# Kernel optimization log

Hardware: AMD Instinct MI355X
Metric: run time of the kernel (lower is better)

Reference implementation:

```python
import jax, jax.numpy as jnp
import numpy as np

B, S, VOCAB, HID, NH, L, SPAN = 4, 512, 25, 512, 8, 12, 512
HEAD = HID // NH
FF = 4 * HID
EPS = 1e-7  # DebertaV2 layer_norm_eps


def _ln(x, g, b):
    m = x.mean(-1, keepdims=True)
    v = ((x - m) ** 2).mean(-1, keepdims=True)
    return (x - m) / jnp.sqrt(v + EPS) * g + b


def setup_inputs() -> dict:
    key = jax.random.key(0)
    ks = iter(jax.random.split(key, 16))
    w = lambda shape: jax.random.normal(next(ks), shape, jnp.float32) * 0.05
    return {
        "x": jax.random.randint(next(ks), (B, S), 0, VOCAB),
        "attention_mask": jnp.ones((B, S), jnp.int32),
        "word_emb": w((VOCAB, HID)),
        "emb_ln_g": jnp.ones((HID,), jnp.float32),
        "emb_ln_b": jnp.zeros((HID,), jnp.float32),
        "rel_emb": w((2 * SPAN, HID)),
        "Wq": w((L, HID, HID)), "bq": jnp.zeros((L, HID), jnp.float32),
        "Wk": w((L, HID, HID)), "bk": jnp.zeros((L, HID), jnp.float32),
        "Wv": w((L, HID, HID)), "bv": jnp.zeros((L, HID), jnp.float32),
        "Wpk": w((L, HID, HID)), "bpk": jnp.zeros((L, HID), jnp.float32),
        "Wpq": w((L, HID, HID)), "bpq": jnp.zeros((L, HID), jnp.float32),
        "Wo": w((L, HID, HID)), "bo": jnp.zeros((L, HID), jnp.float32),
        "ln1_g": jnp.ones((L, HID), jnp.float32), "ln1_b": jnp.zeros((L, HID), jnp.float32),
        "W1": w((L, HID, FF)), "b1": jnp.zeros((L, FF), jnp.float32),
        "W2": w((L, FF, HID)), "b2": jnp.zeros((L, HID), jnp.float32),
        "ln2_g": jnp.ones((L, HID), jnp.float32), "ln2_b": jnp.zeros((L, HID), jnp.float32),
        "cls_w": w((VOCAB, HID)), "cls_b": jnp.zeros((VOCAB,), jnp.float32),
    }


def _forward(x, attention_mask, word_emb, emb_ln_g, emb_ln_b, rel_emb,
             Wq, bq, Wk, bk, Wv, bv, Wpk, bpk, Wpq, bpq, Wo, bo,
             ln1_g, ln1_b, W1, b1, W2, b2, ln2_g, ln2_b, cls_w, cls_b):
    mask = attention_mask.astype(jnp.float32)
    # embeddings: word only (position_biased_input=False), LN, then masked
    h = _ln(word_emb[x], emb_ln_g, emb_ln_b) * mask[..., None]

    rel = jnp.arange(S)[:, None] - jnp.arange(S)[None, :]          # q_pos - k_pos
    c2p_idx = jnp.clip(rel + SPAN, 0, 2 * SPAN - 1)[None, None]    # [1,1,S,S]
    p2c_idx = jnp.clip(-rel + SPAN, 0, 2 * SPAN - 1)[None, None]
    attm = (mask[:, None, None, :] * mask[:, None, :, None]) > 0   # [B,1,S,S]
    scale = jnp.sqrt(jnp.float32(HEAD * 3))                        # scale_factor = 1 + len(pos_att_type)
    neg = jnp.finfo(jnp.float32).min

    def heads(t):  # [B,S,HID] -> [B,NH,S,HEAD]
        return t.reshape(B, S, NH, HEAD).transpose(0, 2, 1, 3)

    for l in range(L):
        q = heads(h @ Wq[l] + bq[l])
        k = heads(h @ Wk[l] + bk[l])
        v = heads(h @ Wv[l] + bv[l])
        # projected relative-position embeddings: [NH, 2*SPAN, HEAD]
        pk = (rel_emb @ Wpk[l] + bpk[l]).reshape(2 * SPAN, NH, HEAD).transpose(1, 0, 2)
        pq = (rel_emb @ Wpq[l] + bpq[l]).reshape(2 * SPAN, NH, HEAD).transpose(1, 0, 2)

        scores = jnp.einsum('bhqd,bhkd->bhqk', q, k)
        # c2p: query content vs key position, gathered at clamp(rel+span)
        c2p = jnp.take_along_axis(jnp.einsum('bhqd,hpd->bhqp', q, pk), c2p_idx, axis=-1)
        # p2c: key content vs query position, gathered at clamp(-rel+span) then transposed
        p2c = jnp.take_along_axis(jnp.einsum('bhkd,hpd->bhkp', k, pq), p2c_idx, axis=-1)
        scores = (scores + c2p + jnp.swapaxes(p2c, -1, -2)) / scale

        scores = jnp.where(attm, scores, neg)
        probs = jnp.where(attm, jax.nn.softmax(scores, axis=-1), 0.0)  # XSoftmax
        ctx = jnp.einsum('bhqk,bhkd->bhqd', probs, v).transpose(0, 2, 1, 3).reshape(B, S, HID)
        h = _ln(ctx @ Wo[l] + bo[l] + h, ln1_g[l], ln1_b[l])
        f = jax.nn.gelu(h @ W1[l] + b1[l], approximate=False) @ W2[l] + b2[l]
        h = _ln(f + h, ln2_g[l], ln2_b[l])

    logits = h @ cls_w.T + cls_b
    return h, logits


def reference(x, attention_mask, word_emb, emb_ln_g, emb_ln_b, rel_emb,
              Wq, bq, Wk, bk, Wv, bv, Wpk, bpk, Wpq, bpq, Wo, bo,
              ln1_g, ln1_b, W1, b1, W2, b2, ln2_g, ln2_b, cls_w, cls_b):
    return _forward(x, attention_mask, word_emb, emb_ln_g, emb_ln_b, rel_emb,
                    Wq, bq, Wk, bk, Wv, bv, Wpk, bpk, Wpq, bpq, Wo, bo,
                    ln1_g, ln1_b, W1, b1, W2, b2, ln2_g, ln2_b, cls_w, cls_b)
```

## Files before the change

### kernel.cpp

```cpp
#include <hip/hip_runtime.h>
#include <hip/hip_bf16.h>

#define BATCH  4
#define SEQ    512
#define TOK    (BATCH*SEQ)
#define HID    512
#define NHEAD  8
#define HEAD   64
#define FFDIM  2048
#define NLAYER 12
#define SPAN2  1024
#define VOCAB  25
#define LNEPS  1e-7f
#define NEG_BIG -3.0e38f

typedef __attribute__((ext_vector_type(8))) short bf16x8;
typedef __attribute__((ext_vector_type(4))) float floatx4;

#define MFMA16(a, b, c) __builtin_amdgcn_mfma_f32_16x16x32_bf16((a), (b), (c), 0, 0, 0)

__device__ __forceinline__ float b2f(unsigned short u) {
    return __uint_as_float(((unsigned int)u) << 16);
}
__device__ __forceinline__ unsigned short f2b(float f) {
    __hip_bfloat16 h = __float2bfloat16(f);
    return *(unsigned short*)&h;
}

__device__ __forceinline__ float block_reduce_sum(float v, float* red) {
    int tid = threadIdx.x;
    red[tid] = v; __syncthreads();
    for (int s = 128; s > 0; s >>= 1) { if (tid < s) red[tid] += red[tid + s]; __syncthreads(); }
    float r = red[0]; __syncthreads();
    return r;
}

__global__ void embed_ln_kernel(const int* __restrict__ x, const int* __restrict__ am,
                                const float* __restrict__ word_emb,
                                const float* __restrict__ g, const float* __restrict__ bb,
                                float* __restrict__ h, unsigned short* __restrict__ hb) {
    __shared__ float red[256];
    int t = blockIdx.x, tid = threadIdx.x;
    const float* we = word_emb + (size_t)x[t] * HID;
    float v1 = we[tid], v2 = we[tid + 256];
    float mean = block_reduce_sum(v1 + v2, red) * (1.0f / HID);
    float d1 = v1 - mean, d2 = v2 - mean;
    float var = block_reduce_sum(d1 * d1 + d2 * d2, red) * (1.0f / HID);
    float rstd = rsqrtf(var + LNEPS);
    float maskf = (float)am[t];
    size_t base = (size_t)t * HID;
    float o1 = (d1 * rstd * g[tid]       + bb[tid])       * maskf;
    float o2 = (d2 * rstd * g[tid + 256] + bb[tid + 256]) * maskf;
    h[base + tid] = o1;        h[base + tid + 256] = o2;
    hb[base + tid] = f2b(o1);  hb[base + tid + 256] = f2b(o2);
}

__global__ void add_ln_kernel(const float* __restrict__ tmp,
                              const float* __restrict__ g, const float* __restrict__ bb,
                              float* __restrict__ h, unsigned short* __restrict__ hb) {
    __shared__ float red[256];
    int t = blockIdx.x, tid = threadIdx.x;
    size_t base = (size_t)t * HID;
    float v1 = tmp[base + tid] + h[base + tid];
    float v2 = tmp[base + tid + 256] + h[base + tid + 256];
    float mean = block_reduce_sum(v1 + v2, red) * (1.0f / HID);
    float d1 = v1 - mean, d2 = v2 - mean;
    float var = block_reduce_sum(d1 * d1 + d2 * d2, red) * (1.0f / HID);
    float rstd = rsqrtf(var + LNEPS);
    float o1 = d1 * rstd * g[tid]       + bb[tid];
    float o2 = d2 * rstd * g[tid + 256] + bb[tid + 256];
    h[base + tid] = o1;        h[base + tid + 256] = o2;
    hb[base + tid] = f2b(o1);  hb[base + tid + 256] = f2b(o2);
}

__global__ void add_ln2_kernel(const float* __restrict__ t1a, const float* __restrict__ t1b,
                               const float* __restrict__ g, const float* __restrict__ bb,
                               float* __restrict__ h, unsigned short* __restrict__ hb) {
    __shared__ float red[256];
    int t = blockIdx.x, tid = threadIdx.x;
    size_t base = (size_t)t * HID;
    float v1 = t1a[base + tid] + t1b[base + tid] + h[base + tid];
    float v2 = t1a[base + tid + 256] + t1b[base + tid + 256] + h[base + tid + 256];
    float mean = block_reduce_sum(v1 + v2, red) * (1.0f / HID);
    float d1 = v1 - mean, d2 = v2 - mean;
    float var = block_reduce_sum(d1 * d1 + d2 * d2, red) * (1.0f / HID);
    float rstd = rsqrtf(var + LNEPS);
    float o1 = d1 * rstd * g[tid]       + bb[tid];
    float o2 = d2 * rstd * g[tid + 256] + bb[tid + 256];
    h[base + tid] = o1;        h[base + tid + 256] = o2;
    hb[base + tid] = f2b(o1);  hb[base + tid + 256] = f2b(o2);
}

__global__ void cvt_rel_kernel(const float* __restrict__ in, unsigned short* __restrict__ out) {
    int i = (blockIdx.x * 256 + threadIdx.x) * 4;
    float4 v = *(const float4*)(in + i);
    out[i] = f2b(v.x); out[i+1] = f2b(v.y); out[i+2] = f2b(v.z); out[i+3] = f2b(v.w);
}

__global__ void tcvt_kernel(const float* __restrict__ in, unsigned short* __restrict__ out,
                            int K, int N) {
    __shared__ float tile[32][33];
    int l = blockIdx.z;
    const float* ip = in + (size_t)l * K * N;
    unsigned short* op = out + (size_t)l * K * N;
    int kb = blockIdx.y * 32, nb = blockIdx.x * 32;
    int tx = threadIdx.x, ty = threadIdx.y;
    #pragma unroll
    for (int i = 0; i < 32; i += 8) tile[ty + i][tx] = ip[(size_t)(kb + ty + i) * N + nb + tx];
    __syncthreads();
    #pragma unroll
    for (int i = 0; i < 32; i += 8) op[(size_t)(nb + ty + i) * K + kb + tx] = f2b(tile[tx][ty + i]);
}

__global__ void tcvt6_kernel(const float* __restrict__ Wq, const float* __restrict__ Wk,
                             const float* __restrict__ Wv, const float* __restrict__ Wpk,
                             const float* __restrict__ Wpq, const float* __restrict__ Wo,
                             unsigned short* __restrict__ out) {
    __shared__ float tile[32][33];
    int z = blockIdx.z, l = z / 6, w = z - l * 6;
    const float* src = w == 0 ? Wq : w == 1 ? Wk : w == 2 ? Wv : w == 3 ? Wpk : w == 4 ? Wpq : Wo;
    const float* ip = src + (size_t)l * HID * HID;
    unsigned short* op = out + ((size_t)w * NLAYER + l) * HID * HID;
    int kb = blockIdx.y * 32, nb = blockIdx.x * 32;
    int tx = threadIdx.x, ty = threadIdx.y;
    #pragma unroll
    for (int i = 0; i < 32; i += 8) tile[ty + i][tx] = ip[(size_t)(kb + ty + i) * HID + nb + tx];
    __syncthreads();
    #pragma unroll
    for (int i = 0; i < 32; i += 8) op[(size_t)(nb + ty + i) * HID + kb + tx] = f2b(tile[tx][ty + i]);
}

__device__ __forceinline__ void gemm_tile_bt(
    const unsigned short* __restrict__ A, const unsigned short* __restrict__ Bt,
    int row0, int col0, int K, int kbeg, int kend,
    floatx4 (&acc)[2][2], unsigned short (&As)[64][72], unsigned short (&Bs)[64][72]) {
    int tid = threadIdx.x;
    int lane = tid & 63, wid = tid >> 6;
    int wm = wid >> 1, wn = wid & 1;
    int m16 = lane & 15, quad = lane >> 4;
    int sr = tid >> 2, sc = (tid & 3) << 4;
    const unsigned short* Ag = A + (size_t)(row0 + sr) * K + sc;
    const unsigned short* Bg = Bt + (size_t)(col0 + sr) * K + sc;
    for (int k0 = kbeg; k0 < kend; k0 += 64) {
        uint4 av0 = *(const uint4*)(Ag + k0);
        uint4 av1 = *(const uint4*)(Ag + k0 + 8);
        uint4 bv0 = *(const uint4*)(Bg + k0);
        uint4 bv1 = *(const uint4*)(Bg + k0 + 8);
        *(uint4*)&As[sr][sc]     = av0;
        *(uint4*)&As[sr][sc + 8] = av1;
        *(uint4*)&Bs[sr][sc]     = bv0;
        *(uint4*)&Bs[sr][sc + 8] = bv1;
        __syncthreads();
        #pragma unroll
        for (int kk = 0; kk < 2; kk++) {
            bf16x8 a0 = *(const bf16x8*)&As[wm * 32 + m16][kk * 32 + quad * 8];
            bf16x8 a1 = *(const bf16x8*)&As[wm * 32 + 16 + m16][kk * 32 + quad * 8];
            bf16x8 b0 = *(const bf16x8*)&Bs[wn * 32 + m16][kk * 32 + quad * 8];
            bf16x8 b1 = *(const bf16x8*)&Bs[wn * 32 + 16 + m16][kk * 32 + quad * 8];
            acc[0][0] = MFMA16(a0, b0, acc[0][0]);
            acc[0][1] = MFMA16(a0, b1, acc[0][1]);
            acc[1][0] = MFMA16(a1, b0, acc[1][0]);
            acc[1][1] = MFMA16(a1, b1, acc[1][1]);
        }
        __syncthreads();
    }
}

template<bool OUT_BF16, bool GELU, int SPLITK>
__global__ __launch_bounds__(256) void gemm_bt(
    const unsigned short* __restrict__ A, const unsigned short* __restrict__ Bt,
    const float* __restrict__ bias, void* __restrict__ Cp, int N, int K) {
    __shared__ unsigned short As[64][72], Bs[64][72];
    int row0 = blockIdx.y * 64, col0 = blockIdx.x * 64;
    int kseg = K / SPLITK;
    int kbeg = kseg * blockIdx.z, kend = kbeg + kseg;
    floatx4 acc[2][2];
    #pragma unroll
    for (int mi = 0; mi < 2; mi++)
        #pragma unroll
        for (int ni = 0; ni < 2; ni++) acc[mi][ni] = (floatx4){0.f, 0.f, 0.f, 0.f};
    gemm_tile_bt(A, Bt, row0, col0, K, kbeg, kend, acc, As, Bs);

    int tid = threadIdx.x, lane = tid & 63, wid = tid >> 6;
    int wm = wid >> 1, wn = wid & 1, m16 = lane & 15, quad = lane >> 4;
    size_t outoff = (size_t)blockIdx.z * (size_t)(gridDim.y << 6) * N;
    #pragma unroll
    for (int ni = 0; ni < 2; ni++) {
        int colg = col0 + wn * 32 + ni * 16 + m16;
        float bval = (SPLITK == 1 || blockIdx.z == 0) ? bias[colg] : 0.0f;
        #pragma unroll
        for (int mi = 0; mi < 2; mi++) {
            #pragma unroll
            for (int r = 0; r < 4; r++) {
                int rowg = row0 + wm * 32 + mi * 16 + quad * 4 + r;
                float v = acc[mi][ni][r] + bval;
                if (GELU) v = 0.5f * v * (1.0f + erff(v * 0.70710678118654752f));
                if (OUT_BF16) ((unsigned short*)Cp)[(size_t)rowg * N + colg] = f2b(v);
                else          ((float*)Cp)[outoff + (size_t)rowg * N + colg] = v;
            }
        }
    }
}

__global__ __launch_bounds__(256) void qkvp_gemm(
    const unsigned short* __restrict__ hb, const unsigned short* __restrict__ relb,
    const unsigned short* __restrict__ Wqt, const unsigned short* __restrict__ Wkt,
    const unsigned short* __restrict__ Wvt, const unsigned short* __restrict__ Wpkt,
    const unsigned short* __restrict__ Wpqt,
    const float* __restrict__ bq, const float* __restrict__ bk, const float* __restrict__ bv,
    const float* __restrict__ bpk, const float* __restrict__ bpq,
    unsigned short* __restrict__ qb, unsigned short* __restrict__ kb,
    unsigned short* __restrict__ vb, unsigned short* __restrict__ pkb,
    unsigned short* __restrict__ pqb) {
    __shared__ unsigned short As[64][72], Bs[64][72];
    int gid = blockIdx.x;
    const unsigned short* A; const unsigned short* Bt; const float* bias; unsigned short* C;
    int trow, tcol;
    if (gid < 768) {
        int op = gid >> 8, t = gid & 255;
        trow = t >> 3; tcol = t & 7;
        A = hb;
        Bt   = op == 0 ? Wqt : op == 1 ? Wkt : Wvt;
        bias = op == 0 ? bq  : op == 1 ? bk  : bv;
        C    = op == 0 ? qb  : op == 1 ? kb  : vb;
    } else {
        int g = gid - 768, op = g >> 7, t = g & 127;
        trow = t >> 3; tcol = t & 7;
        A = relb;
        Bt   = op ? Wpqt : Wpkt;
        bias = op ? bpq  : bpk;
        C    = op ? pqb  : pkb;
    }
    floatx4 acc[2][2];
    #pragma unroll
    for (int mi = 0; mi < 2; mi++)
        #pragma unroll
        for (int ni = 0; ni < 2; ni++) acc[mi][ni] = (floatx4){0.f, 0.f, 0.f, 0.f};
    gemm_tile_bt(A, Bt, trow * 64, tcol * 64, HID, 0, HID, acc, As, Bs);

    int tid = threadIdx.x, lane = tid & 63, wid = tid >> 6;
    int wm = wid >> 1, wn = wid & 1, m16 = lane & 15, quad = lane >> 4;
    #pragma unroll
    for (int ni = 0; ni < 2; ni++) {
        int colg = tcol * 64 + wn * 32 + ni * 16 + m16;
        float bval = bias[colg];
        #pragma unroll
        for (int mi = 0; mi < 2; mi++) {
            #pragma unroll
            for (int r = 0; r < 4; r++) {
                int rowg = trow * 64 + wm * 32 + mi * 16 + quad * 4 + r;
                C[(size_t)rowg * HID + colg] = f2b(acc[mi][ni][r] + bval);
            }
        }
    }
}

template<bool OUT_BF16, bool GELU>
__global__ __launch_bounds__(256) void mfma_gemm(
    const unsigned short* __restrict__ A, const float* __restrict__ B,
    const float* __restrict__ bias, void* __restrict__ Cp, int N, int K) {
    __shared__ unsigned short As[64][72];
    __shared__ unsigned short Bs[64][72];
    int tid = threadIdx.x;
    int lane = tid & 63, wid = tid >> 6;
    int wm = wid >> 1, wn = wid & 1;
    int row0 = blockIdx.y * 64, col0 = blockIdx.x * 64;
    int m16 = lane & 15, quad = lane >> 4;

    int ar = tid >> 2, ac = (tid & 3) << 4;
    int bk = (tid >> 3) << 1, bn = (tid & 7) << 3;

    const unsigned short* Ag = A + (size_t)(row0 + ar) * K + ac;
    const float* Bg = B + (size_t)bk * N + col0 + bn;

    floatx4 acc[2][2];
    #pragma unroll
    for (int mi = 0; mi < 2; mi++)
        #pragma unroll
        for (int ni = 0; ni < 2; ni++) acc[mi][ni] = (floatx4){0.f, 0.f, 0.f, 0.f};

    for (int k0 = 0; k0 < K; k0 += 64) {
        uint4 av0 = *(const uint4*)(Ag + k0);
        uint4 av1 = *(const uint4*)(Ag + k0 + 8);
        const float* br0 = Bg + (size_t)k0 * N;
        const float* br1 = br0 + N;
        float4 b00 = *(const float4*)br0, b01 = *(const float4*)(br0 + 4);
        float4 b10 = *(const float4*)br1, b11 = *(const float4*)(br1 + 4);
        *(uint4*)&As[ar][ac] = av0;
        *(uint4*)&As[ar][ac + 8] = av1;
        float lo[8] = {b00.x, b00.y, b00.z, b00.w, b01.x, b01.y, b01.z, b01.w};
        float hi[8] = {b10.x, b10.y, b10.z, b10.w, b11.x, b11.y, b11.z, b11.w};
        #pragma unroll
        for (int i = 0; i < 8; i++) {
            unsigned int p = (unsigned int)f2b(lo[i]) | ((unsigned int)f2b(hi[i]) << 16);
            *(unsigned int*)&Bs[bn + i][bk] = p;
        }
        __syncthreads();
        #pragma unroll
        for (int kk = 0; kk < 2; kk++) {
            bf16x8 a0 = *(const bf16x8*)&As[wm * 32 + m16][kk * 32 + quad * 8];
            bf16x8 a1 = *(const bf16x8*)&As[wm * 32 + 16 + m16][kk * 32 + quad * 8];
            bf16x8 b0 = *(const bf16x8*)&Bs[wn * 32 + m16][kk * 32 + quad * 8];
            bf16x8 b1 = *(const bf16x8*)&Bs[wn * 32 + 16 + m16][kk * 32 + quad * 8];
            acc[0][0] = MFMA16(a0, b0, acc[0][0]);
            acc[0][1] = MFMA16(a0, b1, acc[0][1]);
            acc[1][0] = MFMA16(a1, b0, acc[1][0]);
            acc[1][1] = MFMA16(a1, b1, acc[1][1]);
        }
        __syncthreads();
    }
    #pragma unroll
    for (int ni = 0; ni < 2; ni++) {
        int colg = col0 + wn * 32 + ni * 16 + m16;
        float bv = bias[colg];
        #pragma unroll
        for (int mi = 0; mi < 2; mi++) {
            #pragma unroll
            for (int r = 0; r < 4; r++) {
                int rowg = row0 + wm * 32 + mi * 16 + quad * 4 + r;
                float v = acc[mi][ni][r] + bv;
                if (GELU) v = 0.5f * v * (1.0f + erff(v * 0.70710678118654752f));
                if (OUT_BF16) ((unsigned short*)Cp)[(size_t)rowg * N + colg] = f2b(v);
                else          ((float*)Cp)[(size_t)rowg * N + colg] = v;
            }
        }
    }
}

__global__ __launch_bounds__(256) void attn_kernel(
    const unsigned short* __restrict__ Q, const unsigned short* __restrict__ K,
    const unsigned short* __restrict__ V,
    const unsigned short* __restrict__ PK, const unsigned short* __restrict__ PQ,
    const int* __restrict__ am, unsigned short* __restrict__ ctx) {
    __shared__ unsigned short Qs[32][72], Ks[32][72];
    __shared__ unsigned short PKw[64][72], PQw[64][72];
    __shared__ unsigned short Vt[64][40];
    __shared__ unsigned short Pls[32][40];
    __shared__ float Afs[32][65];
    __shared__ float Bfs[32][66];
    __shared__ float Scomb[32][33];
    __shared__ float mrow[32], lrow[32], arow[32];
    __shared__ int mkk[32], mq[32];

    int bh = blockIdx.y, b = bh >> 3, hh = bh & 7;
    int q0 = blockIdx.x * 32;
    int tid = threadIdx.x;
    int lane = tid & 63, wave = tid >> 6;
    int quad = lane >> 4, m16 = lane & 15;
    int qt = wave >> 1, kt = wave & 1;
    const float inv_scale = 0.07216878364870323f;

    {
        int r = tid >> 3, c = (tid & 7) * 8;
        *(uint4*)&Qs[r][c] = *(const uint4*)(Q + (size_t)(b * SEQ + q0 + r) * HID + hh * HEAD + c);
        if (tid < 32) { mrow[tid] = NEG_BIG; lrow[tid] = 0.0f; mq[tid] = am[b * SEQ + q0 + tid]; }
    }
    floatx4 accO[2];
    accO[0] = (floatx4){0.f, 0.f, 0.f, 0.f};
    accO[1] = (floatx4){0.f, 0.f, 0.f, 0.f};

    for (int k0 = 0; k0 < SEQ; k0 += 32) {
        __syncthreads();
        {
            int r = tid >> 3, c = (tid & 7) * 8;
            *(uint4*)&Ks[r][c] = *(const uint4*)(K + (size_t)(b * SEQ + k0 + r) * HID + hh * HEAD + c);
            uint4 vv = *(const uint4*)(V + (size_t)(b * SEQ + k0 + r) * HID + hh * HEAD + c);
            unsigned short* vp = (unsigned short*)&vv;
            #pragma unroll
            for (int j = 0; j < 8; j++) Vt[c + j][r] = vp[j];
            int d0 = q0 - k0 + 481;
            #pragma unroll
            for (int i = 0; i < 2; i++) {
                int rr = r + i * 32;
                int row = d0 + rr; row = row > 1023 ? 1023 : row;
                *(uint4*)&PKw[rr][c] = *(const uint4*)(PK + (size_t)row * HID + hh * HEAD + c);
                *(uint4*)&PQw[rr][c] = *(const uint4*)(PQ + (size_t)row * HID + hh * HEAD + c);
            }
            if (tid < 32) mkk[tid] = am[b * SEQ + k0 + tid];
        }
        __syncthreads();

        floatx4 accA0 = (floatx4){0.f,0.f,0.f,0.f}, accA1 = (floatx4){0.f,0.f,0.f,0.f};
        floatx4 accB0 = (floatx4){0.f,0.f,0.f,0.f}, accB1 = (floatx4){0.f,0.f,0.f,0.f};
        floatx4 accS  = (floatx4){0.f,0.f,0.f,0.f};
        #pragma unroll
        for (int ks = 0; ks < 2; ks++) {
            int co = ks * 32 + quad * 8;
            bf16x8 qf0 = *(const bf16x8*)&Qs[m16][co];
            bf16x8 qf1 = *(const bf16x8*)&Qs[16 + m16][co];
            bf16x8 kf0 = *(const bf16x8*)&Ks[m16][co];
            bf16x8 kf1 = *(const bf16x8*)&Ks[16 + m16][co];
            bf16x8 pkf = *(const bf16x8*)&PKw[wave * 16 + m16][co];
            bf16x8 pqf = *(const bf16x8*)&PQw[wave * 16 + m16][co];
            accA0 = MFMA16(qf0, pkf, accA0);
            accA1 = MFMA16(qf1, pkf, accA1);
            accB0 = MFMA16(kf0, pqf, accB0);
            accB1 = MFMA16(kf1, pqf, accB1);
            accS  = MFMA16(qt ? qf1 : qf0, kt ? kf1 : kf0, accS);
        }
        #pragma unroll
        for (int r = 0; r < 4; r++) {
            Afs[quad * 4 + r][wave * 16 + m16]      = accA0[r];
            Afs[16 + quad * 4 + r][wave * 16 + m16] = accA1[r];
            Bfs[quad * 4 + r][wave * 16 + m16]      = accB0[r];
            Bfs[16 + quad * 4 + r][wave * 16 + m16] = accB1[r];
        }
        __syncthreads();

        {
            int kc = kt * 16 + m16;
            #pragma unroll
            for (int r = 0; r < 4; r++) {
                int qq = qt * 16 + quad * 4 + r;
                int j = qq - kc + 31;
                Scomb[qq][kc] = (accS[r] + Afs[qq][j] + Bfs[kc][j]) * inv_scale;
            }
        }
        __syncthreads();

        {
            int r = tid >> 3, cg = (tid & 7) * 4;
            float sv[4]; float tmax = NEG_BIG;
            #pragma unroll
            for (int j = 0; j < 4; j++) {
                sv[j] = mkk[cg + j] ? Scomb[r][cg + j] : NEG_BIG;
                tmax = fmaxf(tmax, sv[j]);
            }
            tmax = fmaxf(tmax, __shfl_xor(tmax, 1));
            tmax = fmaxf(tmax, __shfl_xor(tmax, 2));
            tmax = fmaxf(tmax, __shfl_xor(tmax, 4));
            float mold = mrow[r];
            float mnew = fmaxf(mold, tmax);
            float psum = 0.0f;
            #pragma unroll
            for (int j = 0; j < 4; j++) {
                float p = (sv[j] > -1.5e38f) ? __expf(sv[j] - mnew) : 0.0f;
                unsigned short pb = f2b(p);
                Pls[r][cg + j] = pb;
                psum += b2f(pb);
            }
            psum += __shfl_xor(psum, 1);
            psum += __shfl_xor(psum, 2);
            psum += __shfl_xor(psum, 4);
            if ((tid & 7) == 0) {
                float alpha = __expf(mold - mnew);
                mrow[r] = mnew;
                lrow[r] = lrow[r] * alpha + psum;
                arow[r] = alpha;
            }
        }
        __syncthreads();

        {
            #pragma unroll
            for (int q2 = 0; q2 < 2; q2++) {
                #pragma unroll
                for (int r = 0; r < 4; r++) accO[q2][r] *= arow[q2 * 16 + quad * 4 + r];
            }
            bf16x8 pf0 = *(const bf16x8*)&Pls[m16][quad * 8];
            bf16x8 pf1 = *(const bf16x8*)&Pls[16 + m16][quad * 8];
            bf16x8 vf  = *(const bf16x8*)&Vt[wave * 16 + m16][quad * 8];
            accO[0] = MFMA16(pf0, vf, accO[0]);
            accO[1] = MFMA16(pf1, vf, accO[1]);
        }
    }
    __syncthreads();
    #pragma unroll
    for (int q2 = 0; q2 < 2; q2++) {
        #pragma unroll
        for (int r = 0; r < 4; r++) {
            int qq = q2 * 16 + quad * 4 + r;
            float l = lrow[qq];
            float inv = l > 0.0f ? 1.0f / l : 0.0f;
            inv *= (float)mq[qq];
            ctx[(size_t)(b * SEQ + q0 + qq) * HID + hh * HEAD + wave * 16 + m16] = f2b(accO[q2][r] * inv);
        }
    }
}

__global__ void copy_f_kernel(const float* __restrict__ in, float* __restrict__ out, int n) {
    int i = blockIdx.x * 256 + threadIdx.x;
    if (i < n) out[i] = in[i];
}
__global__ void cls_kernel(const float* __restrict__ h, const float* __restrict__ cls_w,
                           const float* __restrict__ cls_b, float* __restrict__ out) {
    int t = blockIdx.x, v = threadIdx.x;
    if (v < VOCAB) {
        const float* hr = h + (size_t)t * HID;
        const float* wr = cls_w + (size_t)v * HID;
        float acc = cls_b[v];
        for (int d = 0; d < HID; d++) acc += hr[d] * wr[d];
        out[t * VOCAB + v] = acc;
    }
}

extern "C" void kernel_launch(void* const* d_in, const int* in_sizes, int n_in,
                              void* d_out, int out_size, void* d_ws, size_t ws_size,
                              hipStream_t stream) {
    const int* x     = (const int*)d_in[0];
    const int* am    = (const int*)d_in[1];
    const float* word_emb = (const float*)d_in[2];
    const float* emb_g    = (const float*)d_in[3];
    const float* emb_b    = (const float*)d_in[4];
    const float* rel_emb  = (const float*)d_in[5];
    const float* Wq  = (const float*)d_in[6];  const float* bq  = (const float*)d_in[7];
    const float* Wk  = (const float*)d_in[8];  const float* bk  = (const float*)d_in[9];
    const float* Wv  = (const float*)d_in[10]; const float* bv  = (const float*)d_in[11];
    const float* Wpk = (const float*)d_in[12]; const float* bpk = (const float*)d_in[13];
    const float* Wpq = (const float*)d_in[14]; const float* bpq = (const float*)d_in[15];
    const float* Wo  = (const float*)d_in[16]; const float* bo  = (const float*)d_in[17];
    const float* ln1g = (const float*)d_in[18]; const float* ln1b = (const float*)d_in[19];
    const float* W1  = (const float*)d_in[20]; const float* b1  = (const float*)d_in[21];
    const float* W2  = (const float*)d_in[22]; const float* b2  = (const float*)d_in[23];
    const float* ln2g = (const float*)d_in[24]; const float* ln2b = (const float*)d_in[25];
    const float* cls_w = (const float*)d_in[26]; const float* cls_b = (const float*)d_in[27];

    char* wsb = (char*)d_ws;
    const size_t NEED_BIG = 107u << 20;

    if (ws_size >= NEED_BIG) {
        float* h  = (float*)wsb;
        float* t1 = (float*)(wsb + (4u << 20));
        float* t2 = (float*)(wsb + (8u << 20));
        unsigned short* qb   = (unsigned short*)(wsb + (12u << 20));
        unsigned short* kb   = (unsigned short*)(wsb + (14u << 20));
        unsigned short* vb   = (unsigned short*)(wsb + (16u << 20));
        unsigned short* pkb  = (unsigned short*)(wsb + (18u << 20));
        unsigned short* pqb  = (unsigned short*)(wsb + (19u << 20));
        unsigned short* relb = (unsigned short*)(wsb + (20u << 20));
        unsigned short* hb   = (unsigned short*)(wsb + (21u << 20));
        unsigned short* ctx  = hb;
        unsigned short* ffb  = qb;
        unsigned short* Wqt  = (unsigned short*)(wsb + (23u << 20));
        unsigned short* W1t  = (unsigned short*)(wsb + (59u << 20));
        unsigned short* W2t  = (unsigned short*)(wsb + (83u << 20));

        const size_t M512 = (size_t)HID * HID;

        tcvt6_kernel<<<dim3(16, 16, 72), dim3(32, 8), 0, stream>>>(Wq, Wk, Wv, Wpk, Wpq, Wo, Wqt);
        tcvt_kernel<<<dim3(64, 16, 12), dim3(32, 8), 0, stream>>>(W1, W1t, HID, FFDIM);
        tcvt_kernel<<<dim3(16, 64, 12), dim3(32, 8), 0, stream>>>(W2, W2t, FFDIM, HID);
        cvt_rel_kernel<<<dim3(SPAN2 * HID / 1024), dim3(256), 0, stream>>>(rel_emb, relb);
        embed_ln_kernel<<<dim3(TOK), dim3(256), 0, stream>>>(x, am, word_emb, emb_g, emb_b, h, hb);

        for (int l = 0; l < NLAYER; l++) {
            qkvp_gemm<<<dim3(1024), dim3(256), 0, stream>>>(
                hb, relb,
                Wqt + (size_t)(0 * NLAYER + l) * M512, Wqt + (size_t)(1 * NLAYER + l) * M512,
                Wqt + (size_t)(2 * NLAYER + l) * M512, Wqt + (size_t)(3 * NLAYER + l) * M512,
                Wqt + (size_t)(4 * NLAYER + l) * M512,
                bq + l * HID, bk + l * HID, bv + l * HID, bpk + l * HID, bpq + l * HID,
                qb, kb, vb, pkb, pqb);

            attn_kernel<<<dim3(SEQ / 32, BATCH * NHEAD), dim3(256), 0, stream>>>(
                qb, kb, vb, pkb, pqb, am, ctx);

            gemm_bt<false, false, 2><<<dim3(HID / 64, TOK / 64, 2), dim3(256), 0, stream>>>(
                ctx, Wqt + (size_t)(5 * NLAYER + l) * M512, bo + l * HID, t1, HID, HID);
            add_ln2_kernel<<<dim3(TOK), dim3(256), 0, stream>>>(t1, t2, ln1g + l * HID, ln1b + l * HID, h, hb);

            gemm_bt<true, true, 1><<<dim3(FFDIM / 64, TOK / 64, 1), dim3(256), 0, stream>>>(
                hb, W1t + (size_t)l * HID * FFDIM, b1 + l * FFDIM, ffb, FFDIM, HID);
            gemm_bt<false, false, 2><<<dim3(HID / 64, TOK / 64, 2), dim3(256), 0, stream>>>(
                ffb, W2t + (size_t)l * HID * FFDIM, b2 + l * HID, t1, HID, FFDIM);
            add_ln2_kernel<<<dim3(TOK), dim3(256), 0, stream>>>(t1, t2, ln2g + l * HID, ln2b + l * HID, h, hb);
        }

        float* out_f = (float*)d_out;
        copy_f_kernel<<<dim3(TOK * HID / 256), dim3(256), 0, stream>>>(h, out_f, TOK * HID);
        cls_kernel<<<dim3(TOK), dim3(32), 0, stream>>>(h, cls_w, cls_b, out_f + TOK * HID);
        return;
    }

    const size_t NEEDED = 19u << 20;
    if (ws_size < NEEDED) return;
    float* h  = (float*)wsb;
    float* t1 = (float*)(wsb + (4u << 20));
    unsigned short* qb   = (unsigned short*)(wsb + (8u << 20));
    unsigned short* kb   = qb  + (1u << 20);
    unsigned short* vb   = kb  + (1u << 20);
    unsigned short* pkb  = vb  + (1u << 20);
    unsigned short* pqb  = pkb + (1u << 19);
    unsigned short* relb = (unsigned short*)(wsb + (16u << 20));
    unsigned short* hb   = (unsigned short*)(wsb + (17u << 20));
    unsigned short* ctx  = hb;
    unsigned short* ffb  = qb;

    cvt_rel_kernel<<<dim3(SPAN2 * HID / 1024), dim3(256), 0, stream>>>(rel_emb, relb);
    embed_ln_kernel<<<dim3(TOK), dim3(256), 0, stream>>>(x, am, word_emb, emb_g, emb_b, h, hb);

    for (int l = 0; l < NLAYER; l++) {
        const float* Wq_l = Wq + (size_t)l * HID * HID;
        const float* Wk_l = Wk + (size_t)l * HID * HID;
        const float* Wv_l = Wv + (size_t)l * HID * HID;
        const float* Wo_l = Wo + (size_t)l * HID * HID;
        const float* Wpk_l = Wpk + (size_t)l * HID * HID;
        const float* Wpq_l = Wpq + (size_t)l * HID * HID;
        const float* W1_l = W1 + (size_t)l * HID * FFDIM;
        const float* W2_l = W2 + (size_t)l * FFDIM * HID;

        mfma_gemm<true,  false><<<dim3(HID/64, TOK/64),   dim3(256), 0, stream>>>(hb,   Wq_l,  bq + l*HID,  qb,  HID, HID);
        mfma_gemm<true,  false><<<dim3(HID/64, TOK/64),   dim3(256), 0, stream>>>(hb,   Wk_l,  bk + l*HID,  kb,  HID, HID);
        mfma_gemm<true,  false><<<dim3(HID/64, TOK/64),   dim3(256), 0, stream>>>(hb,   Wv_l,  bv + l*HID,  vb,  HID, HID);
        mfma_gemm<true,  false><<<dim3(HID/64, SPAN2/64), dim3(256), 0, stream>>>(relb, Wpk_l, bpk + l*HID, pkb, HID, HID);
        mfma_gemm<true,  false><<<dim3(HID/64, SPAN2/64), dim3(256), 0, stream>>>(relb, Wpq_l, bpq + l*HID, pqb, HID, HID);

        attn_kernel<<<dim3(SEQ/32, BATCH*NHEAD), dim3(256), 0, stream>>>(qb, kb, vb, pkb, pqb, am, ctx);

        mfma_gemm<false, false><<<dim3(HID/64, TOK/64),   dim3(256), 0, stream>>>(ctx,  Wo_l,  bo + l*HID,  t1,  HID, HID);
        add_ln_kernel<<<dim3(TOK), dim3(256), 0, stream>>>(t1, ln1g + l*HID, ln1b + l*HID, h, hb);

        mfma_gemm<true,  true ><<<dim3(FFDIM/64, TOK/64), dim3(256), 0, stream>>>(hb,   W1_l,  b1 + l*FFDIM, ffb, FFDIM, HID);
        mfma_gemm<false, false><<<dim3(HID/64, TOK/64),   dim3(256), 0, stream>>>(ffb,  W2_l,  b2 + l*HID,  t1,  HID, FFDIM);
        add_ln_kernel<<<dim3(TOK), dim3(256), 0, stream>>>(t1, ln2g + l*HID, ln2b + l*HID, h, hb);
    }

    float* out_f = (float*)d_out;
    copy_f_kernel<<<dim3(TOK*HID/256), dim3(256), 0, stream>>>(h, out_f, TOK*HID);
    cls_kernel<<<dim3(TOK), dim3(32), 0, stream>>>(h, cls_w, cls_b, out_f + TOK*HID);
}
```

Before: 1.508 ms.

## Restructure attention kernel into per-wave split-K flash attention with register softmax

The attention kernel now gives each wave a 16-query row block and one of two interleaved key-tile streams (split-K). Q fragments and relative-position PK/PQ fragments are loaded straight into registers, and softmax statistics are kept per wave in registers with shuffle reductions. This removes most of the block-wide __syncthreads and the shared Scomb/mrow/lrow staging of the old version. The two key streams are merged at the end through shared memory, V is stored transposed with an XOR swizzle to avoid bank conflicts, and launch bounds ask for two blocks per SM. In exchange each wave recomputes overlapping position-bias tiles (3 tiles instead of 2), holds more registers, and needs a final merge step.

```diff
diff --git a/kernel.cpp b/kernel.cpp
--- a/kernel.cpp
+++ b/kernel.cpp
@@ -327,153 +327,224 @@
     }
 }
 
-__global__ __launch_bounds__(256) void attn_kernel(
+__global__ __launch_bounds__(256, 2) void attn_kernel(
     const unsigned short* __restrict__ Q, const unsigned short* __restrict__ K,
     const unsigned short* __restrict__ V,
     const unsigned short* __restrict__ PK, const unsigned short* __restrict__ PQ,
     const int* __restrict__ am, unsigned short* __restrict__ ctx) {
-    __shared__ unsigned short Qs[32][72], Ks[32][72];
-    __shared__ unsigned short PKw[64][72], PQw[64][72];
-    __shared__ unsigned short Vt[64][40];
-    __shared__ unsigned short Pls[32][40];
-    __shared__ float Afs[32][65];
-    __shared__ float Bfs[32][66];
-    __shared__ float Scomb[32][33];
-    __shared__ float mrow[32], lrow[32], arow[32];
-    __shared__ int mkk[32], mq[32];
+    __shared__ unsigned short Ks[2][32][72];
+    __shared__ unsigned short Vt[2][64][40];
+    __shared__ float Afs[4][16][49];
+    __shared__ float Bfs[4][32][50];
+    __shared__ unsigned short Pls[4][16][40];
+    __shared__ int mkk[2][32];
+    __shared__ float mergeML[2][2][16];
 
     int bh = blockIdx.y, b = bh >> 3, hh = bh & 7;
     int q0 = blockIdx.x * 32;
     int tid = threadIdx.x;
     int lane = tid & 63, wave = tid >> 6;
+    int u = wave >> 1;
+    int s = wave & 1;
     int quad = lane >> 4, m16 = lane & 15;
-    int qt = wave >> 1, kt = wave & 1;
     const float inv_scale = 0.07216878364870323f;
 
-    {
-        int r = tid >> 3, c = (tid & 7) * 8;
-        *(uint4*)&Qs[r][c] = *(const uint4*)(Q + (size_t)(b * SEQ + q0 + r) * HID + hh * HEAD + c);
-        if (tid < 32) { mrow[tid] = NEG_BIG; lrow[tid] = 0.0f; mq[tid] = am[b * SEQ + q0 + tid]; }
-    }
-    floatx4 accO[2];
-    accO[0] = (floatx4){0.f, 0.f, 0.f, 0.f};
-    accO[1] = (floatx4){0.f, 0.f, 0.f, 0.f};
-
-    for (int k0 = 0; k0 < SEQ; k0 += 32) {
+    const unsigned short* qg = Q + (size_t)(b * SEQ + q0 + u * 16 + m16) * HID + hh * HEAD;
+    bf16x8 qf0 = *(const bf16x8*)(qg + quad * 8);
+    bf16x8 qf1 = *(const bf16x8*)(qg + 32 + quad * 8);
+
+    int sr = tid >> 3;
+    int sc = (tid & 7) * 8;
+    int vkey = ((sc >> 3) & 3) << 3;
+
+    floatx4 accO[4];
+    #pragma unroll
+    for (int nt = 0; nt < 4; nt++) accO[nt] = (floatx4){0.f, 0.f, 0.f, 0.f};
+    float mreg[4] = {NEG_BIG, NEG_BIG, NEG_BIG, NEG_BIG};
+    float lreg[4] = {0.f, 0.f, 0.f, 0.f};
+
+    for (int ph = 0; ph < 8; ph++) {
+        int t = 2 * ph + s;
+        int P0  = q0 - 32 * t + 481;
+        int P20 = 32 * t - q0 + 481;
+        int Jb  = 16 - 16 * u;
+
+        bf16x8 pkf[3][2], pqf[3][2];
+        #pragma unroll
+        for (int nt = 0; nt < 3; nt++) {
+            int prow = P0 + 16 * u + nt * 16 + m16;
+            const unsigned short* pg = PK + (size_t)prow * HID + hh * HEAD + quad * 8;
+            pkf[nt][0] = *(const bf16x8*)pg;
+            pkf[nt][1] = *(const bf16x8*)(pg + 32);
+            int prow2 = P20 + Jb + nt * 16 + m16;
+            if (prow2 > 1023) prow2 = 1023;
+            const unsigned short* pg2 = PQ + (size_t)prow2 * HID + hh * HEAD + quad * 8;
+            pqf[nt][0] = *(const bf16x8*)pg2;
+            pqf[nt][1] = *(const bf16x8*)(pg2 + 32);
+        }
+
+        #pragma unroll
+        for (int sl = 0; sl < 2; sl++) {
+            int k0 = ph * 64 + sl * 32;
+            const unsigned short* kg = K + (size_t)(b * SEQ + k0 + sr) * HID + hh * HEAD + sc;
+            *(uint4*)&Ks[sl][sr][sc] = *(const uint4*)kg;
+            uint4 vv = *(const uint4*)(V + (size_t)(b * SEQ + k0 + sr) * HID + hh * HEAD + sc);
+            unsigned short* vp = (unsigned short*)&vv;
+            #pragma unroll
+            for (int j = 0; j < 8; j++) Vt[sl][sc + j][sr ^ vkey] = vp[j];
+        }
+        if (tid < 64) mkk[tid >> 5][tid & 31] = am[b * SEQ + ph * 64 + tid];
         __syncthreads();
+
+        floatx4 accS[2];
+        accS[0] = (floatx4){0.f, 0.f, 0.f, 0.f};
+        accS[1] = (floatx4){0.f, 0.f, 0.f, 0.f};
+        #pragma unroll
+        for (int n = 0; n < 2; n++) {
+            bf16x8 kfa = *(const bf16x8*)&Ks[s][n * 16 + m16][quad * 8];
+            bf16x8 kfb = *(const bf16x8*)&Ks[s][n * 16 + m16][32 + quad * 8];
+            accS[n] = MFMA16(qf0, kfa, accS[n]);
+            accS[n] = MFMA16(qf1, kfb, accS[n]);
+        }
+
         {
-            int r = tid >> 3, c = (tid & 7) * 8;
-            *(uint4*)&Ks[r][c] = *(const uint4*)(K + (size_t)(b * SEQ + k0 + r) * HID + hh * HEAD + c);
-            uint4 vv = *(const uint4*)(V + (size_t)(b * SEQ + k0 + r) * HID + hh * HEAD + c);
-            unsigned short* vp = (unsigned short*)&vv;
-            #pragma unroll
-            for (int j = 0; j < 8; j++) Vt[c + j][r] = vp[j];
-            int d0 = q0 - k0 + 481;
-            #pragma unroll
-            for (int i = 0; i < 2; i++) {
-                int rr = r + i * 32;
-                int row = d0 + rr; row = row > 1023 ? 1023 : row;
-                *(uint4*)&PKw[rr][c] = *(const uint4*)(PK + (size_t)row * HID + hh * HEAD + c);
-                *(uint4*)&PQw[rr][c] = *(const uint4*)(PQ + (size_t)row * HID + hh * HEAD + c);
-            }
-            if (tid < 32) mkk[tid] = am[b * SEQ + k0 + tid];
+            floatx4 accA[3];
+            #pragma unroll
+            for (int nt = 0; nt < 3; nt++) {
+                accA[nt] = (floatx4){0.f, 0.f, 0.f, 0.f};
+                accA[nt] = MFMA16(qf0, pkf[nt][0], accA[nt]);
+                accA[nt] = MFMA16(qf1, pkf[nt][1], accA[nt]);
+            }
+            #pragma unroll
+            for (int nt = 0; nt < 3; nt++)
+                #pragma unroll
+                for (int r = 0; r < 4; r++)
+                    Afs[wave][quad * 4 + r][nt * 16 + m16] = accA[nt][r];
+        }
+
+        {
+            floatx4 accB[2][3];
+            #pragma unroll
+            for (int mt = 0; mt < 2; mt++) {
+                bf16x8 afa = *(const bf16x8*)&Ks[s][mt * 16 + m16][quad * 8];
+                bf16x8 afb = *(const bf16x8*)&Ks[s][mt * 16 + m16][32 + quad * 8];
+                #pragma unroll
+                for (int nt = 0; nt < 3; nt++) {
+                    accB[mt][nt] = (floatx4){0.f, 0.f, 0.f, 0.f};
+                    accB[mt][nt] = MFMA16(afa, pqf[nt][0], accB[mt][nt]);
+                    accB[mt][nt] = MFMA16(afb, pqf[nt][1], accB[mt][nt]);
+                }
+            }
+            #pragma unroll
+            for (int mt = 0; mt < 2; mt++)
+                #pragma unroll
+                for (int nt = 0; nt < 3; nt++)
+                    #pragma unroll
+                    for (int r = 0; r < 4; r++)
+                        Bfs[wave][mt * 16 + quad * 4 + r][nt * 16 + m16] = accB[mt][nt][r];
+        }
+
+        float sv[2][4];
+        float tmax[4] = {NEG_BIG, NEG_BIG, NEG_BIG, NEG_BIG};
+        #pragma unroll
+        for (int n = 0; n < 2; n++) {
+            #pragma unroll
+            for (int r = 0; r < 4; r++) {
+                int qq = quad * 4 + r;
+                int kc = n * 16 + m16;
+                float av = Afs[wave][qq][qq - kc + 31];
+                float bv = Bfs[wave][kc][kc - qq + 15];
+                float x = (accS[n][r] + av + bv) * inv_scale;
+                x = mkk[s][kc] ? x : NEG_BIG;
+                sv[n][r] = x;
+                tmax[r] = fmaxf(tmax[r], x);
+            }
+        }
+        float alpha[4], psum[4];
+        #pragma unroll
+        for (int r = 0; r < 4; r++) {
+            float tm = tmax[r];
+            tm = fmaxf(tm, __shfl_xor(tm, 1));
+            tm = fmaxf(tm, __shfl_xor(tm, 2));
+            tm = fmaxf(tm, __shfl_xor(tm, 4));
+            tm = fmaxf(tm, __shfl_xor(tm, 8));
+            float mo = mreg[r];
+            float mn = fmaxf(mo, tm);
+            alpha[r] = __expf(mo - mn);
+            mreg[r] = mn;
+        }
+        #pragma unroll
+        for (int r = 0; r < 4; r++) psum[r] = 0.f;
+        #pragma unroll
+        for (int n = 0; n < 2; n++) {
+            #pragma unroll
+            for (int r = 0; r < 4; r++) {
+                float p = (sv[n][r] > -1.5e38f) ? __expf(sv[n][r] - mreg[r]) : 0.0f;
+                unsigned short pb = f2b(p);
+                Pls[wave][quad * 4 + r][n * 16 + m16] = pb;
+                psum[r] += b2f(pb);
+            }
+        }
+        #pragma unroll
+        for (int r = 0; r < 4; r++) {
+            float ps = psum[r];
+            ps += __shfl_xor(ps, 1);
+            ps += __shfl_xor(ps, 2);
+            ps += __shfl_xor(ps, 4);
+            ps += __shfl_xor(ps, 8);
+            lreg[r] = lreg[r] * alpha[r] + ps;
+        }
+        #pragma unroll
+        for (int nt = 0; nt < 4; nt++)
+            #pragma unroll
+            for (int r = 0; r < 4; r++) accO[nt][r] *= alpha[r];
+        {
+            bf16x8 pf = *(const bf16x8*)&Pls[wave][m16][quad * 8];
+            #pragma unroll
+            for (int nt = 0; nt < 4; nt++) {
+                int d = nt * 16 + m16;
+                int kq = (quad ^ ((d >> 3) & 3)) * 8;
+                bf16x8 vf = *(const bf16x8*)&Vt[s][d][kq];
+                accO[nt] = MFMA16(pf, vf, accO[nt]);
+            }
         }
         __syncthreads();
-
-        floatx4 accA0 = (floatx4){0.f,0.f,0.f,0.f}, accA1 = (floatx4){0.f,0.f,0.f,0.f};
-        floatx4 accB0 = (floatx4){0.f,0.f,0.f,0.f}, accB1 = (floatx4){0.f,0.f,0.f,0.f};
-        floatx4 accS  = (floatx4){0.f,0.f,0.f,0.f};
-        #pragma unroll
-        for (int ks = 0; ks < 2; ks++) {
-            int co = ks * 32 + quad * 8;
-            bf16x8 qf0 = *(const bf16x8*)&Qs[m16][co];
-            bf16x8 qf1 = *(const bf16x8*)&Qs[16 + m16][co];
-            bf16x8 kf0 = *(const bf16x8*)&Ks[m16][co];
-            bf16x8 kf1 = *(const bf16x8*)&Ks[16 + m16][co];
-            bf16x8 pkf = *(const bf16x8*)&PKw[wave * 16 + m16][co];
-            bf16x8 pqf = *(const bf16x8*)&PQw[wave * 16 + m16][co];
-            accA0 = MFMA16(qf0, pkf, accA0);
-            accA1 = MFMA16(qf1, pkf, accA1);
-            accB0 = MFMA16(kf0, pqf, accB0);
-            accB1 = MFMA16(kf1, pqf, accB1);
-            accS  = MFMA16(qt ? qf1 : qf0, kt ? kf1 : kf0, accS);
-        }
+    }
+
+    __syncthreads();
+    float* mo = &Bfs[0][0][0];
+    if (s == 1) {
+        #pragma unroll
+        for (int nt = 0; nt < 4; nt++)
+            #pragma unroll
+            for (int r = 0; r < 4; r++)
+                mo[u * 1056 + (quad * 4 + r) * 66 + nt * 16 + m16] = accO[nt][r];
+        if (m16 == 0) {
+            #pragma unroll
+            for (int r = 0; r < 4; r++) {
+                mergeML[u][0][quad * 4 + r] = mreg[r];
+                mergeML[u][1][quad * 4 + r] = lreg[r];
+            }
+        }
+    }
+    __syncthreads();
+    if (s == 0) {
         #pragma unroll
         for (int r = 0; r < 4; r++) {
-            Afs[quad * 4 + r][wave * 16 + m16]      = accA0[r];
-            Afs[16 + quad * 4 + r][wave * 16 + m16] = accA1[r];
-            Bfs[quad * 4 + r][wave * 16 + m16]      = accB0[r];
-            Bfs[16 + quad * 4 + r][wave * 16 + m16] = accB1[r];
-        }
-        __syncthreads();
-
-        {
-            int kc = kt * 16 + m16;
-            #pragma unroll
-            for (int r = 0; r < 4; r++) {
-                int qq = qt * 16 + quad * 4 + r;
-                int j = qq - kc + 31;
-                Scomb[qq][kc] = (accS[r] + Afs[qq][j] + Bfs[kc][j]) * inv_scale;
-            }
-        }
-        __syncthreads();
-
-        {
-            int r = tid >> 3, cg = (tid & 7) * 4;
-            float sv[4]; float tmax = NEG_BIG;
-            #pragma unroll
-            for (int j = 0; j < 4; j++) {
-                sv[j] = mkk[cg + j] ? Scomb[r][cg + j] : NEG_BIG;
-                tmax = fmaxf(tmax, sv[j]);
-            }
-            tmax = fmaxf(tmax, __shfl_xor(tmax, 1));
-            tmax = fmaxf(tmax, __shfl_xor(tmax, 2));
-            tmax = fmaxf(tmax, __shfl_xor(tmax, 4));
-            float mold = mrow[r];
-            float mnew = fmaxf(mold, tmax);
-            float psum = 0.0f;
-            #pragma unroll
-            for (int j = 0; j < 4; j++) {
-                float p = (sv[j] > -1.5e38f) ? __expf(sv[j] - mnew) : 0.0f;
-                unsigned short pb = f2b(p);
-                Pls[r][cg + j] = pb;
-                psum += b2f(pb);
-            }
-            psum += __shfl_xor(psum, 1);
-            psum += __shfl_xor(psum, 2);
-            psum += __shfl_xor(psum, 4);
-            if ((tid & 7) == 0) {
-                float alpha = __expf(mold - mnew);
-                mrow[r] = mnew;
-                lrow[r] = lrow[r] * alpha + psum;
-                arow[r] = alpha;
-            }
-        }
-        __syncthreads();
-
-        {
-            #pragma unroll
-            for (int q2 = 0; q2 < 2; q2++) {
-                #pragma unroll
-                for (int r = 0; r < 4; r++) accO[q2][r] *= arow[q2 * 16 + quad * 4 + r];
-            }
-            bf16x8 pf0 = *(const bf16x8*)&Pls[m16][quad * 8];
-            bf16x8 pf1 = *(const bf16x8*)&Pls[16 + m16][quad * 8];
-            bf16x8 vf  = *(const bf16x8*)&Vt[wave * 16 + m16][quad * 8];
-            accO[0] = MFMA16(pf0, vf, accO[0]);
-            accO[1] = MFMA16(pf1, vf, accO[1]);
-        }
-    }
-    __syncthreads();
-    #pragma unroll
-    for (int q2 = 0; q2 < 2; q2++) {
-        #pragma unroll
-        for (int r = 0; r < 4; r++) {
-            int qq = q2 * 16 + quad * 4 + r;
-            float l = lrow[qq];
-            float inv = l > 0.0f ? 1.0f / l : 0.0f;
-            inv *= (float)mq[qq];
-            ctx[(size_t)(b * SEQ + q0 + qq) * HID + hh * HEAD + wave * 16 + m16] = f2b(accO[q2][r] * inv);
+            int row = quad * 4 + r;
+            float m1 = mergeML[u][0][row], l1 = mergeML[u][1][row];
+            float m0 = mreg[r], l0 = lreg[r];
+            float mt = fmaxf(m0, m1);
+            float a0 = __expf(m0 - mt), a1 = __expf(m1 - mt);
+            float lt = l0 * a0 + l1 * a1;
+            float inv = lt > 0.0f ? 1.0f / lt : 0.0f;
+            inv *= (float)am[b * SEQ + q0 + u * 16 + row];
+            #pragma unroll
+            for (int nt = 0; nt < 4; nt++) {
+                float o1 = mo[u * 1056 + row * 66 + nt * 16 + m16];
+                float val = (accO[nt][r] * a0 + o1 * a1) * inv;
+                ctx[(size_t)(b * SEQ + q0 + u * 16 + row) * HID + hh * HEAD + nt * 16 + m16] = f2b(val);
+            }
         }
     }
 }
```

Measured after the change: 1.456 ms. 1.04x faster.
